# Performance work log

Measured on AMD Instinct MI355X. Metric: run time of the kernel, lower is better.

The kernel has to match this reference:

```python
import jax, jax.numpy as jnp
import numpy as np
import math

D_MODEL = 256
D_STATE = 16
D_CONV = 4
EXPAND = 2
N_HEADS = 4
D_INNER = EXPAND * D_MODEL          # 512
DT_RANK = (D_MODEL + 15) // 16      # 16
B_SZ, SEQ = 4, 2048


def setup_inputs() -> dict:
    key = jax.random.key(0)
    ks = jax.random.split(key, 12)
    rn = lambda i, shp, sc=0.02: jax.random.normal(ks[i], shp, dtype=jnp.float32) * sc
    x = jax.random.normal(ks[0], (B_SZ, SEQ, D_MODEL), dtype=jnp.float32)
    return dict(
        x=x,
        ln_g=jnp.ones((D_MODEL,), jnp.float32),
        ln_b=jnp.zeros((D_MODEL,), jnp.float32),
        W_in=rn(1, (D_MODEL, 2 * D_INNER)),
        conv_w=rn(2, (D_INNER, D_CONV), 0.1),
        conv_b=jnp.zeros((D_INNER,), jnp.float32),
        W_xproj=rn(3, (D_INNER, DT_RANK + 2 * D_STATE)),
        W_dt=rn(4, (DT_RANK, D_INNER), 0.1),
        b_dt=jnp.full((D_INNER,), -4.6, jnp.float32),  # softplus ~ 0.01 init
        A_log=jnp.log(jnp.tile(jnp.arange(1, D_STATE + 1, dtype=jnp.float32), (D_INNER, 1))),
        Dp=jnp.ones((D_INNER,), jnp.float32),
        W_out_m=rn(5, (D_INNER, D_MODEL)),
        W_qkv=rn(6, (D_MODEL, 3 * D_MODEL)),
        b_qkv=jnp.zeros((3 * D_MODEL,), jnp.float32),
        W_o=rn(7, (D_MODEL, D_MODEL)),
        b_o=jnp.zeros((D_MODEL,), jnp.float32),
        W_gate=rn(8, (2 * D_MODEL, D_MODEL)),
        b_gate=jnp.zeros((D_MODEL,), jnp.float32),
    )


def _sssd_forward(x, ln_g, ln_b, W_in, conv_w, conv_b, W_xproj, W_dt, b_dt,
                  A_log, Dp, W_out_m, W_qkv, b_qkv, W_o, b_o, W_gate, b_gate):
    B, L, D = x.shape
    # LayerNorm
    mu = x.mean(-1, keepdims=True)
    var = x.var(-1, keepdims=True)
    xn = (x - mu) * jax.lax.rsqrt(var + 1e-5) * ln_g + ln_b

    # ---- Mamba branch ----
    xz = xn @ W_in                      # (B,L,2*D_INNER)
    xm, z = jnp.split(xz, 2, axis=-1)
    # causal depthwise conv1d (kernel D_CONV)
    xp = jnp.pad(xm, ((0, 0), (D_CONV - 1, 0), (0, 0)))
    xc = conv_b + sum(xp[:, k:k + L, :] * conv_w[:, k] for k in range(D_CONV))
    xc = jax.nn.silu(xc)
    dbl = xc @ W_xproj                  # (B,L,DT_RANK+2*D_STATE)
    dt_in = dbl[..., :DT_RANK]
    Bm = dbl[..., DT_RANK:DT_RANK + D_STATE]
    Cm = dbl[..., DT_RANK + D_STATE:]
    dt = jax.nn.softplus(dt_in @ W_dt + b_dt)   # (B,L,D_INNER)
    A = -jnp.exp(A_log)                 # (D_INNER, D_STATE)

    def step(h, inp):
        x_t, dt_t, B_t, C_t = inp       # (B,Din),(B,Din),(B,N),(B,N)
        dA = jnp.exp(dt_t[..., None] * A)               # (B,Din,N)
        h = dA * h + (dt_t * x_t)[..., None] * B_t[:, None, :]
        y = jnp.einsum('bdn,bn->bd', h, C_t)
        return h, y

    h0 = jnp.zeros((B, D_INNER, D_STATE), x.dtype)
    xs = (jnp.swapaxes(xc, 0, 1), jnp.swapaxes(dt, 0, 1),
          jnp.swapaxes(Bm, 0, 1), jnp.swapaxes(Cm, 0, 1))
    _, ys = jax.lax.scan(step, h0, xs)
    y = jnp.swapaxes(ys, 0, 1) + xc * Dp
    y = y * jax.nn.silu(z)
    ssm_out = y @ W_out_m               # (B,L,D)

    # ---- MHSA branch (eval: no dropout) ----
    hd = D // N_HEADS
    qkv = xn @ W_qkv + b_qkv
    q, k, v = jnp.split(qkv, 3, axis=-1)
    sh = lambda t: t.reshape(B, L, N_HEADS, hd).transpose(0, 2, 1, 3)
    q, k, v = sh(q), sh(k), sh(v)
    scores = jnp.einsum('bhqd,bhkd->bhqk', q, k) * (1.0 / math.sqrt(hd))
    attn = jax.nn.softmax(scores, axis=-1)
    o = jnp.einsum('bhqk,bhkd->bhqd', attn, v).transpose(0, 2, 1, 3).reshape(B, L, D)
    attn_out = o @ W_o + b_o

    # ---- sigmoid gate fusion ----
    gate = jax.nn.sigmoid(jnp.concatenate([ssm_out, attn_out], axis=-1) @ W_gate + b_gate)
    fused = gate * ssm_out + (1.0 - gate) * attn_out
    return x + fused


def reference(x, ln_g, ln_b, W_in, conv_w, conv_b, W_xproj, W_dt, b_dt,
              A_log, Dp, W_out_m, W_qkv, b_qkv, W_o, b_o, W_gate, b_gate):
    return _sssd_forward(x, ln_g, ln_b, W_in, conv_w, conv_b, W_xproj, W_dt, b_dt,
                         A_log, Dp, W_out_m, W_qkv, b_qkv, W_o, b_o, W_gate, b_gate)
```

## Files before the change

kernel.cpp:

```cpp
#include <hip/hip_runtime.h>
#include <math.h>

#define B_SZ 4
#define SEQ 2048
#define DM 256
#define DI 512
#define DS 16
#define DTR 16
#define NH 4
#define HD 64
#define T_TOK (B_SZ*SEQ)
#define NCH 64
#define CL (SEQ/NCH)
#define NSP 4
#define QSCALE 0.18033688f

typedef short bf16x8 __attribute__((ext_vector_type(8)));
typedef float f32x4  __attribute__((ext_vector_type(4)));
typedef float f32x16 __attribute__((ext_vector_type(16)));
typedef unsigned short u16;

__device__ __forceinline__ float sigmoidf_(float x){ return 1.f/(1.f+__expf(-x)); }
__device__ __forceinline__ u16 f2bf(float x){
  unsigned int u = __float_as_uint(x);
  u += 0x7fffu + ((u>>16)&1u);
  return (u16)(u>>16);
}
__device__ __forceinline__ float bf2f(u16 u){ return __uint_as_float(((unsigned)u)<<16); }
__device__ __forceinline__ unsigned cvt_pk_bf16(float lo, float hi){
  unsigned r;
  asm("v_cvt_pk_bf16_f32 %0, %1, %2" : "=v"(r) : "v"(lo), "v"(hi));
  return r;
}
__device__ __forceinline__ void permswap(unsigned &a, unsigned &b){
  asm volatile("v_permlane32_swap_b32 %0, %1" : "+v"(a), "+v"(b));
}
__device__ __forceinline__ float xor32f(float v){
  unsigned a = __float_as_uint(v), b = a;
  permswap(a, b);
  return __uint_as_float(a);
}

struct TcvtArgs {
  const float* src[6];
  u16* dst[6];
  int K[6];
  int Nvalid[6];
  int Npad[6];
};
__global__ __launch_bounds__(256) void tcvt_all(TcvtArgs a) {
  int wi = blockIdx.z;
  int K = a.K[wi], Nv = a.Nvalid[wi], Np = a.Npad[wi];
  int k0 = blockIdx.x*64, n0 = blockIdx.y*64;
  if (k0 >= K || n0 >= Np) return;
  __shared__ u16 tile[64][65];
  const float* src = a.src[wi];
  u16* dst = a.dst[wi];
  int tn = threadIdx.x & 63, tq = threadIdx.x >> 6;
#pragma unroll
  for (int j=0;j<16;++j){
    int kk = j*4 + tq;
    int n = n0 + tn;
    tile[tn][kk] = (n < Nv) ? f2bf(src[(size_t)(k0+kk)*Nv + n]) : (u16)0;
  }
  __syncthreads();
#pragma unroll
  for (int j=0;j<16;++j){
    int nn = j*4 + tq;
    dst[(size_t)(n0+nn)*K + k0 + tn] = tile[nn][tn];
  }
}

__global__ __launch_bounds__(256) void ln_kernel(const float* __restrict__ x,
    const float* __restrict__ g, const float* __restrict__ b,
    u16* __restrict__ xn_bf) {
  int wid = threadIdx.x >> 6;
  int lane = threadIdx.x & 63;
  int token = blockIdx.x*4 + wid;
  const float* xr = x + (size_t)token*DM;
  float4 v = *(const float4*)&xr[lane*4];
  float s  = v.x+v.y+v.z+v.w;
  float ss = v.x*v.x+v.y*v.y+v.z*v.z+v.w*v.w;
  for (int m=1;m<64;m<<=1){ s += __shfl_xor(s,m); ss += __shfl_xor(ss,m); }
  float mu  = s * (1.f/DM);
  float var = ss*(1.f/DM) - mu*mu;
  float rs  = rsqrtf(var + 1e-5f);
  float4 gv = *(const float4*)&g[lane*4];
  float4 bv = *(const float4*)&b[lane*4];
  uint2 o;
  o.x = cvt_pk_bf16((v.x-mu)*rs*gv.x + bv.x, (v.y-mu)*rs*gv.y + bv.y);
  o.y = cvt_pk_bf16((v.z-mu)*rs*gv.z + bv.z, (v.w-mu)*rs*gv.w + bv.w);
  *(uint2*)&xn_bf[(size_t)token*DM + lane*4] = o;
}

template<int ACT>
__global__ __launch_bounds__(256) void gemm_mfma(const u16* __restrict__ A,
    const u16* __restrict__ Wt, const float* __restrict__ bias,
    float* __restrict__ C, u16* __restrict__ Cbf, int K, int ldc, int nvalid,
    int qcols, float qscale, const float* __restrict__ xres,
    const float* __restrict__ cat2, u16* __restrict__ vTout,
    u16* __restrict__ qkvout,
    const u16* __restrict__ A2, const u16* __restrict__ Wt2, int K2,
    const float* __restrict__ bias2) {
  __shared__ u16 lds[12288];
  int tid = threadIdx.x;
  int m0 = blockIdx.y*128;
  int n0 = blockIdx.x*64;
  const u16* Ap = A; const u16* Wp = Wt; int Kp = K; const float* bp = bias;
  int halfsel = 0;
  if (ACT==6){
    halfsel = (blockIdx.x >= 4);
    if (halfsel){ Ap = A2; Wp = Wt2; Kp = K2; bp = bias2; }
    n0 = (blockIdx.x & 3)*64;
  }
  int w = tid>>6, l = tid&63, lq = l&15, lg = l>>4;
  int wm = w>>1, wn = w&1;
  f32x4 acc[4][2] = {};
  for (int k0 = 0; k0 < Kp; k0 += 64) {
#pragma unroll
    for (int i=0;i<4;++i){
      int gid = i*256 + tid;
      int row = gid>>3, g = gid&7;
      *(bf16x8*)&lds[row*64 + ((g ^ (row&7))*8)] =
          *(const bf16x8*)&Ap[(size_t)(m0+row)*Kp + k0 + g*8];
    }
#pragma unroll
    for (int i=0;i<2;++i){
      int gid = i*256 + tid;
      int row = gid>>3, g = gid&7;
      *(bf16x8*)&lds[8192 + row*64 + ((g ^ (row&7))*8)] =
          *(const bf16x8*)&Wp[(size_t)(n0+row)*Kp + k0 + g*8];
    }
    __syncthreads();
#pragma unroll
    for (int ks=0;ks<2;++ks){
      bf16x8 af[4], bfv[2];
#pragma unroll
      for (int mi=0;mi<4;++mi){
        int row = wm*64 + mi*16 + lq;
        af[mi] = *(bf16x8*)&lds[row*64 + (((ks*4+lg) ^ (row&7))*8)];
      }
#pragma unroll
      for (int nj=0;nj<2;++nj){
        int row = wn*32 + nj*16 + lq;
        bfv[nj] = *(bf16x8*)&lds[8192 + row*64 + (((ks*4+lg) ^ (row&7))*8)];
      }
#pragma unroll
      for (int mi=0;mi<4;++mi)
#pragma unroll
        for (int nj=0;nj<2;++nj)
          acc[mi][nj] = __builtin_amdgcn_mfma_f32_16x16x32_bf16(af[mi], bfv[nj], acc[mi][nj], 0,0,0);
    }
    __syncthreads();
  }
#pragma unroll
  for (int mi=0;mi<4;++mi){
#pragma unroll
    for (int nj=0;nj<2;++nj){
#pragma unroll
      for (int r=0;r<4;++r){
        int row = m0 + wm*64 + mi*16 + lg*4 + r;
        int col = n0 + wn*32 + nj*16 + lq;
        if (col < nvalid) {
          float v = acc[mi][nj][r];
          if (ACT==0 && bias) v += bias[col];
          if (col < qcols) v *= qscale;
          if (ACT==2) {
            if (bias) v += bias[col];
            float g = sigmoidf_(v);
            float sv = cat2[(size_t)row*512 + col];
            float av = cat2[(size_t)row*512 + 256 + col];
            C[(size_t)row*256 + col] = xres[(size_t)row*256 + col] + g*sv + (1.f-g)*av;
          } else if (ACT==5) {
            if (col < 1024) {
              Cbf[(size_t)row*1024 + col] = f2bf(v);
            } else {
              int c2 = col - 1024;
              v += bias[c2];
              if (c2 < 256) v *= qscale;
              qkvout[(size_t)row*768 + c2] = f2bf(v);
              if (c2 >= 512) {
                int bb = row>>11, ll = row&2047;
                int hh = (c2-512)>>6, dd = (c2-512)&63;
                vTout[(((size_t)(bb*4+hh))*64 + dd)*SEQ + ll] = f2bf(v);
              }
            }
          } else if (ACT==6) {
            if (bp) v += bp[col];
            C[(size_t)row*512 + halfsel*256 + col] = v;
            Cbf[(size_t)row*512 + halfsel*256 + col] = f2bf(v);
          } else {
            if (C)   C[(size_t)row*ldc + col] = v;
            if (Cbf) Cbf[(size_t)row*ldc + col] = f2bf(v);
          }
        }
      }
    }
  }
}

__global__ __launch_bounds__(256) void conv_kernel(const u16* __restrict__ xzb,
    const float* __restrict__ cw, const float* __restrict__ cb,
    u16* __restrict__ xc_bf) {
  int idx = blockIdx.x*256 + threadIdx.x;
  int d2 = (idx & 255)*2;
  int t = idx >> 8;
  int l = t & (SEQ-1);
  float acc0 = cb[d2], acc1 = cb[d2+1];
  float4 wA = *(const float4*)&cw[d2*4];
  float4 wB = *(const float4*)&cw[d2*4+4];
  const u16* base = xzb + (size_t)t*1024 + d2;
  ushort2 v;
  if (l>=3){ v = *(const ushort2*)&base[-3*1024]; acc0 += bf2f(v.x)*wA.x; acc1 += bf2f(v.y)*wB.x; }
  if (l>=2){ v = *(const ushort2*)&base[-2*1024]; acc0 += bf2f(v.x)*wA.y; acc1 += bf2f(v.y)*wB.y; }
  if (l>=1){ v = *(const ushort2*)&base[-1*1024]; acc0 += bf2f(v.x)*wA.z; acc1 += bf2f(v.y)*wB.z; }
  v = *(const ushort2*)&base[0];
  acc0 += bf2f(v.x)*wA.w; acc1 += bf2f(v.y)*wB.w;
  float r0 = acc0 * sigmoidf_(acc0);
  float r1 = acc1 * sigmoidf_(acc1);
  *(unsigned*)&xc_bf[(size_t)t*DI + d2] = cvt_pk_bf16(r0, r1);
}

__global__ __launch_bounds__(256) void dt_kernel(const float* __restrict__ dbl,
    const float* __restrict__ Wdt, const float* __restrict__ bdt,
    u16* __restrict__ dt) {
  __shared__ float sdbl[4][16];
  int wid = threadIdx.x>>6, lane = threadIdx.x&63;
  int token = blockIdx.x*4 + wid;
  if (lane < 16) sdbl[wid][lane] = dbl[(size_t)token*48 + lane];
  __syncthreads();
  float din[16];
#pragma unroll
  for (int k=0;k<16;++k) din[k] = sdbl[wid][k];
#pragma unroll
  for (int r=0;r<8;++r){
    int d = lane + r*64;
    float acc = bdt[d];
#pragma unroll
    for (int k=0;k<16;++k) acc += din[k]*Wdt[k*DI+d];
    float sp = (acc > 20.f) ? acc : log1pf(__expf(acc));
    dt[(size_t)token*DI+d] = f2bf(sp);
  }
}

__global__ __launch_bounds__(512) void scan_p1(const u16* __restrict__ xc_bf,
    const u16* __restrict__ dt, const float* __restrict__ dbl,
    const float* __restrict__ A_log, u16* __restrict__ Pws, u16* __restrict__ Hws) {
  __shared__ float sB[CL][16];
  int d = threadIdx.x;
  int bc = blockIdx.x;
  int b = bc >> 6, c = bc & 63;
  {
    int t = threadIdx.x >> 4, n = threadIdx.x & 15;
    sB[t][n] = dbl[((size_t)b*SEQ + c*CL + t)*48 + DTR + n];
  }
  __syncthreads();
  float An[16];
#pragma unroll
  for (int i=0;i<4;++i){
    float4 a = *(const float4*)&A_log[d*16 + i*4];
    An[i*4+0] = -__expf(a.x); An[i*4+1] = -__expf(a.y);
    An[i*4+2] = -__expf(a.z); An[i*4+3] = -__expf(a.w);
  }
  float h[16] = {};
  float P[16];
#pragma unroll
  for (int n=0;n<16;++n) P[n] = 1.f;
  size_t tok = (size_t)b*SEQ + c*CL;
  for (int t=0;t<CL;++t,++tok){
    float dtv = bf2f(dt[tok*DI+d]);
    float xcv = bf2f(xc_bf[tok*DI+d]);
    float u = dtv*xcv;
    float4 B0 = *(float4*)&sB[t][0];
    float4 B1 = *(float4*)&sB[t][4];
    float4 B2 = *(float4*)&sB[t][8];
    float4 B3 = *(float4*)&sB[t][12];
    float Bv[16] = {B0.x,B0.y,B0.z,B0.w,B1.x,B1.y,B1.z,B1.w,
                    B2.x,B2.y,B2.z,B2.w,B3.x,B3.y,B3.z,B3.w};
#pragma unroll
    for (int n=0;n<16;++n){
      float e = __expf(dtv*An[n]);
      P[n] *= e;
      h[n] = e*h[n] + u*Bv[n];
    }
  }
  size_t base = (((size_t)b*NCH + c)*DI + d)*16;
#pragma unroll
  for (int i=0;i<8;++i){
    *(unsigned*)&Pws[base + i*2] = cvt_pk_bf16(P[i*2], P[i*2+1]);
    *(unsigned*)&Hws[base + i*2] = cvt_pk_bf16(h[i*2], h[i*2+1]);
  }
}

__global__ __launch_bounds__(256) void scan_combine(const u16* __restrict__ Pws,
    const u16* __restrict__ Hws, u16* __restrict__ H0ws) {
  int gid = blockIdx.x*256 + threadIdx.x;
  int b  = gid >> 13;
  int dn = gid & 8191;
  float h0 = 0.f;
#pragma unroll 4
  for (int c=0;c<NCH;++c){
    size_t idx = ((size_t)(b*NCH+c)<<13) + dn;
    H0ws[idx] = f2bf(h0);
    h0 = bf2f(Pws[idx])*h0 + bf2f(Hws[idx]);
  }
}

__global__ __launch_bounds__(512) void scan_p2(const u16* __restrict__ xc_bf,
    const u16* __restrict__ dt, const float* __restrict__ dbl,
    const float* __restrict__ A_log, const float* __restrict__ Dp,
    const u16* __restrict__ xzb, const u16* __restrict__ H0ws,
    u16* __restrict__ ygate_bf) {
  __shared__ float sBC[CL][32];
  int d = threadIdx.x;
  int bc = blockIdx.x;
  int b = bc >> 6, c = bc & 63;
#pragma unroll
  for (int i=0;i<2;++i){
    int idx = i*512 + threadIdx.x;
    int t = idx >> 5, q = idx & 31;
    sBC[t][q] = dbl[((size_t)b*SEQ + c*CL + t)*48 + DTR + q];
  }
  __syncthreads();
  float An[16];
#pragma unroll
  for (int i=0;i<4;++i){
    float4 a = *(const float4*)&A_log[d*16 + i*4];
    An[i*4+0] = -__expf(a.x); An[i*4+1] = -__expf(a.y);
    An[i*4+2] = -__expf(a.z); An[i*4+3] = -__expf(a.w);
  }
  float Dd = Dp[d];
  float h[16];
  size_t base = (((size_t)b*NCH + c)*DI + d)*16;
  {
    bf16x8 h8a = *(const bf16x8*)&H0ws[base];
    bf16x8 h8b = *(const bf16x8*)&H0ws[base+8];
#pragma unroll
    for (int n=0;n<8;++n){ h[n] = bf2f((u16)h8a[n]); h[8+n] = bf2f((u16)h8b[n]); }
  }
  size_t tok = (size_t)b*SEQ + c*CL;
  for (int t=0;t<CL;++t,++tok){
    float dtv = bf2f(dt[tok*DI+d]);
    float xcv = bf2f(xc_bf[tok*DI+d]);
    float zv  = bf2f(xzb[tok*1024 + DI + d]);
    float u = dtv*xcv;
    float4 B0 = *(float4*)&sBC[t][0];
    float4 B1 = *(float4*)&sBC[t][4];
    float4 B2 = *(float4*)&sBC[t][8];
    float4 B3 = *(float4*)&sBC[t][12];
    float4 C0 = *(float4*)&sBC[t][16];
    float4 C1 = *(float4*)&sBC[t][20];
    float4 C2 = *(float4*)&sBC[t][24];
    float4 C3 = *(float4*)&sBC[t][28];
    float Bv[16] = {B0.x,B0.y,B0.z,B0.w,B1.x,B1.y,B1.z,B1.w,
                    B2.x,B2.y,B2.z,B2.w,B3.x,B3.y,B3.z,B3.w};
    float Cv[16] = {C0.x,C0.y,C0.z,C0.w,C1.x,C1.y,C1.z,C1.w,
                    C2.x,C2.y,C2.z,C2.w,C3.x,C3.y,C3.z,C3.w};
    float y = 0.f;
#pragma unroll
    for (int n=0;n<16;++n){
      float e = __expf(dtv*An[n]);
      h[n] = e*h[n] + u*Bv[n];
      y += h[n]*Cv[n];
    }
    y += xcv*Dd;
    ygate_bf[tok*DI + d] = f2bf(y * (zv*sigmoidf_(zv)));
  }
}

__global__ __launch_bounds__(256) void attn_mfma_kernel(const u16* __restrict__ qkvb,
    const u16* __restrict__ vT,
    u16* __restrict__ Opart, float* __restrict__ ml) {
  int H = blockIdx.x + 8*blockIdx.y + 128*(int)blockIdx.z;
  int cx = H & 7, kk = H >> 3;
  int xq = kk & 7;
  int G  = cx*8 + (kk >> 3);
  int bh = G & 15, s = G >> 4;
  int b = bh>>2, h = bh&3;
  int tid = threadIdx.x;
  int w = tid>>6, l = tid&63;
  int lo32 = l & 31;
  int hi = l >> 5;
  size_t bbase = (size_t)b*SEQ;
  size_t vbase = (size_t)bh*HD*SEQ;
  int q_base = xq*256 + w*64;

  bf16x8 qf[2][4];
#pragma unroll
  for (int qg=0; qg<2; ++qg)
#pragma unroll
    for (int dsl=0; dsl<4; ++dsl)
      qf[qg][dsl] = *(const bf16x8*)&qkvb[(bbase + q_base + qg*32 + lo32)*768 + h*HD + dsl*16 + hi*8];

  float m_[2] = {-1e30f,-1e30f}, l_[2] = {0.f,0.f};
  f32x16 oacc[2][2] = {};

#define EXCH(X, Y, s_own, s_oth) { \
  unsigned xa = (X), yb = (Y); \
  permswap(xa, yb); \
  s_own = (l < 32) ? (X) : xa; \
  s_oth = (l < 32) ? yb : (Y); }

  for (int kt=s*8; kt<s*8+8; ++kt){
#pragma unroll
    for (int t32=0; t32<2; ++t32){
      const u16* kbase = &qkvb[(bbase + (size_t)kt*64 + t32*32 + lo32)*768 + 256 + h*HD + hi*8];
      bf16x8 kf[4];
#pragma unroll
      for (int dsl=0; dsl<4; ++dsl)
        kf[dsl] = *(const bf16x8*)&kbase[dsl*16];
      const u16* vb0 = &vT[vbase + (size_t)(lo32     )*SEQ + kt*64 + t32*32 + hi*8];
      const u16* vb1 = &vT[vbase + (size_t)(32 + lo32)*SEQ + kt*64 + t32*32 + hi*8];
      bf16x8 vf00 = *(const bf16x8*)&vb0[0];
      bf16x8 vf01 = *(const bf16x8*)&vb0[16];
      bf16x8 vf10 = *(const bf16x8*)&vb1[0];
      bf16x8 vf11 = *(const bf16x8*)&vb1[16];

      bf16x8 pf[2][2];
#pragma unroll
      for (int qg=0; qg<2; ++qg){
        f32x16 sacc = {0,0,0,0,0,0,0,0,0,0,0,0,0,0,0,0};
#pragma unroll
        for (int dsl=0; dsl<4; ++dsl)
          sacc = __builtin_amdgcn_mfma_f32_32x32x16_bf16(kf[dsl], qf[qg][dsl], sacc, 0,0,0);

        float tm = sacc[0];
#pragma unroll
        for (int r=1;r<16;++r) tm = fmaxf(tm, sacc[r]);
        tm = fmaxf(tm, xor32f(tm));
        if (__any(tm - m_[qg] > 8.f)) {
          float mn = fmaxf(m_[qg], tm);
          float sc = exp2f(m_[qg] - mn);
          m_[qg] = mn;
          l_[qg] *= sc;
#pragma unroll
          for (int r=0;r<16;++r){ oacc[qg][0][r] *= sc; oacc[qg][1][r] *= sc; }
        }
        float p[16];
        float ps = 0.f;
#pragma unroll
        for (int r=0;r<16;++r){ p[r] = exp2f(sacc[r] - m_[qg]); ps += p[r]; }
        ps += xor32f(ps);
        l_[qg] += ps;

        unsigned A0 = cvt_pk_bf16(p[0],p[1]),  A1 = cvt_pk_bf16(p[2],p[3]);
        unsigned B0 = cvt_pk_bf16(p[4],p[5]),  B1 = cvt_pk_bf16(p[6],p[7]);
        unsigned C0 = cvt_pk_bf16(p[8],p[9]),  C1 = cvt_pk_bf16(p[10],p[11]);
        unsigned D0 = cvt_pk_bf16(p[12],p[13]),D1 = cvt_pk_bf16(p[14],p[15]);
        unsigned s0,s1,s2,s3,s4,s5,s6,s7;
        EXCH(A0,B0,s0,s2); EXCH(A1,B1,s1,s3);
        EXCH(C0,D0,s4,s6); EXCH(C1,D1,s5,s7);
        ((unsigned*)&pf[qg][0])[0]=s0; ((unsigned*)&pf[qg][0])[1]=s1;
        ((unsigned*)&pf[qg][0])[2]=s2; ((unsigned*)&pf[qg][0])[3]=s3;
        ((unsigned*)&pf[qg][1])[0]=s4; ((unsigned*)&pf[qg][1])[1]=s5;
        ((unsigned*)&pf[qg][1])[2]=s6; ((unsigned*)&pf[qg][1])[3]=s7;
      }

      oacc[0][0] = __builtin_amdgcn_mfma_f32_32x32x16_bf16(vf00, pf[0][0], oacc[0][0], 0,0,0);
      oacc[0][0] = __builtin_amdgcn_mfma_f32_32x32x16_bf16(vf01, pf[0][1], oacc[0][0], 0,0,0);
      oacc[0][1] = __builtin_amdgcn_mfma_f32_32x32x16_bf16(vf10, pf[0][0], oacc[0][1], 0,0,0);
      oacc[0][1] = __builtin_amdgcn_mfma_f32_32x32x16_bf16(vf11, pf[0][1], oacc[0][1], 0,0,0);
      oacc[1][0] = __builtin_amdgcn_mfma_f32_32x32x16_bf16(vf00, pf[1][0], oacc[1][0], 0,0,0);
      oacc[1][0] = __builtin_amdgcn_mfma_f32_32x32x16_bf16(vf01, pf[1][1], oacc[1][0], 0,0,0);
      oacc[1][1] = __builtin_amdgcn_mfma_f32_32x32x16_bf16(vf10, pf[1][0], oacc[1][1], 0,0,0);
      oacc[1][1] = __builtin_amdgcn_mfma_f32_32x32x16_bf16(vf11, pf[1][1], oacc[1][1], 0,0,0);
    }
  }
#undef EXCH

  int sidx = bh*NSP + s;
#pragma unroll
  for (int qg=0; qg<2; ++qg){
    size_t rb = ((size_t)sidx*SEQ + q_base + qg*32 + lo32)*64;
#pragma unroll
    for (int dtile=0; dtile<2; ++dtile){
#pragma unroll
      for (int rg=0; rg<4; ++rg){
        uint2 pk;
        pk.x = cvt_pk_bf16(oacc[qg][dtile][rg*4+0], oacc[qg][dtile][rg*4+1]);
        pk.y = cvt_pk_bf16(oacc[qg][dtile][rg*4+2], oacc[qg][dtile][rg*4+3]);
        *(uint2*)&Opart[rb + dtile*32 + rg*8 + 4*hi] = pk;
      }
    }
    if (l < 32){
      ml[((size_t)sidx*SEQ + q_base + qg*32 + lo32)*2    ] = m_[qg];
      ml[((size_t)sidx*SEQ + q_base + qg*32 + lo32)*2 + 1] = l_[qg];
    }
  }
}

__global__ __launch_bounds__(256) void attn_merge_kernel(const u16* __restrict__ Opart,
    const float* __restrict__ ml, u16* __restrict__ attn_bf) {
  int w = threadIdx.x>>6, lane = threadIdx.x&63;
  int R = blockIdx.x*4 + w;
  int bh = R>>11, q = R&2047;
  float m[NSP], lv[NSP];
#pragma unroll
  for (int s=0;s<NSP;++s){
    m[s]  = ml[((size_t)(bh*NSP+s)*SEQ + q)*2];
    lv[s] = ml[((size_t)(bh*NSP+s)*SEQ + q)*2 + 1];
  }
  float ms = m[0];
#pragma unroll
  for (int s=1;s<NSP;++s) ms = fmaxf(ms, m[s]);
  float o = 0.f, lsum = 0.f;
#pragma unroll
  for (int s=0;s<NSP;++s){
    float wsc = exp2f(m[s]-ms);
    lsum += wsc*lv[s];
    o += wsc*bf2f(Opart[((size_t)(bh*NSP+s)*SEQ + q)*64 + lane]);
  }
  size_t token = (size_t)(bh>>2)*SEQ + q;
  attn_bf[token*DM + (bh&3)*HD + lane] = f2bf(o/lsum);
}

extern "C" void kernel_launch(void* const* d_in, const int* in_sizes, int n_in,
                              void* d_out, int out_size, void* d_ws, size_t ws_size,
                              hipStream_t stream) {
  const float* x      = (const float*)d_in[0];
  const float* ln_g   = (const float*)d_in[1];
  const float* ln_b   = (const float*)d_in[2];
  const float* W_in   = (const float*)d_in[3];
  const float* conv_w = (const float*)d_in[4];
  const float* conv_b = (const float*)d_in[5];
  const float* W_xproj= (const float*)d_in[6];
  const float* W_dt   = (const float*)d_in[7];
  const float* b_dt   = (const float*)d_in[8];
  const float* A_log  = (const float*)d_in[9];
  const float* Dp     = (const float*)d_in[10];
  const float* W_out_m= (const float*)d_in[11];
  const float* W_qkv  = (const float*)d_in[12];
  const float* b_qkv  = (const float*)d_in[13];
  const float* W_o    = (const float*)d_in[14];
  const float* b_o    = (const float*)d_in[15];
  const float* W_gate = (const float*)d_in[16];
  const float* b_gate = (const float*)d_in[17];
  float* out = (float*)d_out;

  float* ws = (float*)d_ws;
  u16*   xn_bf   = (u16*)(ws);
  u16*   xzb     = (u16*)(ws + 1048576);
  u16*   qkv_bf  = (u16*)(ws + 9437184);
  u16*   xc_bf   = (u16*)(ws + 12582912);
  float* dblb    = ws + 16777216;
  u16*   dtb     = (u16*)(ws + 17170432);
  u16*   ygate_bf= (u16*)(ws + 21364736);
  u16*   attn_bf = (u16*)(ws + 23461888);
  float* catb    = ws + 24510464;
  u16*   catb_bf = (u16*)(ws + 28704768);
  float* gateb   = ws + 30801920;
  u16*   Wt_all  = (u16*)(ws + 32899072);
  u16*   Opart = (u16*)(ws + 1048576);
  float* mlb   = (float*)xn_bf;
  u16*   vTb   = (u16*)gateb;
  u16*   Pws   = (u16*)catb;
  u16*   Hws   = (u16*)(catb + 1048576);
  u16*   H0ws  = (u16*)(catb + 2097152);

  u16* Wt_in   = Wt_all;
  u16* Wt_qkv  = Wt_all + 262144;
  u16* Wt_out  = Wt_all + 458752;
  u16* Wt_o    = Wt_all + 589824;
  u16* Wt_gate = Wt_all + 655360;
  u16* Wt_xp   = Wt_all + 786432;

  TcvtArgs ta;
  ta.src[0]=W_in;    ta.dst[0]=Wt_in;   ta.K[0]=256; ta.Nvalid[0]=1024; ta.Npad[0]=1024;
  ta.src[1]=W_qkv;   ta.dst[1]=Wt_qkv;  ta.K[1]=256; ta.Nvalid[1]=768;  ta.Npad[1]=768;
  ta.src[2]=W_out_m; ta.dst[2]=Wt_out;  ta.K[2]=512; ta.Nvalid[2]=256;  ta.Npad[2]=256;
  ta.src[3]=W_o;     ta.dst[3]=Wt_o;    ta.K[3]=256; ta.Nvalid[3]=256;  ta.Npad[3]=256;
  ta.src[4]=W_gate;  ta.dst[4]=Wt_gate; ta.K[4]=512; ta.Nvalid[4]=256;  ta.Npad[4]=256;
  ta.src[5]=W_xproj; ta.dst[5]=Wt_xp;   ta.K[5]=512; ta.Nvalid[5]=48;   ta.Npad[5]=64;
  tcvt_all<<<dim3(8,16,6), 256, 0, stream>>>(ta);

  ln_kernel<<<T_TOK/4, 256, 0, stream>>>(x, ln_g, ln_b, xn_bf);
  gemm_mfma<5><<<dim3(28,64), 256, 0, stream>>>(xn_bf, Wt_in, b_qkv, nullptr, xzb, 256, 0, 1792, 0, QSCALE, nullptr, nullptr, vTb, qkv_bf, nullptr, nullptr, 0, nullptr);
  conv_kernel<<<T_TOK, 256, 0, stream>>>(xzb, conv_w, conv_b, xc_bf);
  gemm_mfma<0><<<dim3(1,64), 256, 0, stream>>>(xc_bf, Wt_xp, nullptr, dblb, nullptr, 512, 48, 48, 0, 1.f, nullptr, nullptr, nullptr, nullptr, nullptr, nullptr, 0, nullptr);
  dt_kernel<<<T_TOK/4, 256, 0, stream>>>(dblb, W_dt, b_dt, dtb);
  scan_p1<<<B_SZ*NCH, 512, 0, stream>>>(xc_bf, dtb, dblb, A_log, Pws, Hws);
  scan_combine<<<128, 256, 0, stream>>>(Pws, Hws, H0ws);
  scan_p2<<<B_SZ*NCH, 512, 0, stream>>>(xc_bf, dtb, dblb, A_log, Dp, xzb, H0ws, ygate_bf);
  attn_mfma_kernel<<<dim3(8, 16, 4), 256, 0, stream>>>(qkv_bf, vTb, Opart, mlb);
  attn_merge_kernel<<<8192, 256, 0, stream>>>(Opart, mlb, attn_bf);
  gemm_mfma<6><<<dim3(8,64), 256, 0, stream>>>(ygate_bf, Wt_out, nullptr, catb, catb_bf, 512, 512, 256, 0, 1.f, nullptr, nullptr, nullptr, nullptr, attn_bf, Wt_o, 256, b_o);
  gemm_mfma<2><<<dim3(4,64), 256, 0, stream>>>(catb_bf, Wt_gate, b_gate, out, nullptr, 512, 256, 256, 0, 1.f, x, catb, nullptr, nullptr, nullptr, nullptr, 0, b_gate);
}
```

Measured before the change: 234.8 us.

## Fuse conv, x-projection and dt into one launch alongside attention

Replaces the separate conv, x-projection GEMM and dt kernels with a single pre-scan stage. Each of 128 blocks handles 64 tokens: it computes the causal conv and SiLU, stages the result in swizzled LDS, runs the x-projection with MFMA, then applies dt-projection and softplus. These blocks run in the same launch as the attention blocks (block index below 128 takes the SSM path), which cuts launch count and lets the SSM preprocessing overlap with attention. The attention partial outputs are moved into the catb workspace, which is only reused later by the scan. The 64KB static LDS array applies to every block, including attention blocks that never use it, which can limit occupancy. The conv loop inside each SSM block is also serial over 64 tokens.

Result: slower. 283.8 us (+20.9%).

```diff
diff --git a/kernel.cpp b/kernel.cpp
--- a/kernel.cpp
+++ b/kernel.cpp
@@ -163,7 +163,6 @@
         int col = n0 + wn*32 + nj*16 + lq;
         if (col < nvalid) {
           float v = acc[mi][nj][r];
-          if (ACT==0 && bias) v += bias[col];
           if (col < qcols) v *= qscale;
           if (ACT==2) {
             if (bias) v += bias[col];
@@ -189,9 +188,6 @@
             if (bp) v += bp[col];
             C[(size_t)row*512 + halfsel*256 + col] = v;
             Cbf[(size_t)row*512 + halfsel*256 + col] = f2bf(v);
-          } else {
-            if (C)   C[(size_t)row*ldc + col] = v;
-            if (Cbf) Cbf[(size_t)row*ldc + col] = f2bf(v);
           }
         }
       }
@@ -199,47 +195,202 @@
   }
 }
 
-__global__ __launch_bounds__(256) void conv_kernel(const u16* __restrict__ xzb,
-    const float* __restrict__ cw, const float* __restrict__ cb,
-    u16* __restrict__ xc_bf) {
-  int idx = blockIdx.x*256 + threadIdx.x;
-  int d2 = (idx & 255)*2;
-  int t = idx >> 8;
-  int l = t & (SEQ-1);
-  float acc0 = cb[d2], acc1 = cb[d2+1];
-  float4 wA = *(const float4*)&cw[d2*4];
-  float4 wB = *(const float4*)&cw[d2*4+4];
-  const u16* base = xzb + (size_t)t*1024 + d2;
-  ushort2 v;
-  if (l>=3){ v = *(const ushort2*)&base[-3*1024]; acc0 += bf2f(v.x)*wA.x; acc1 += bf2f(v.y)*wB.x; }
-  if (l>=2){ v = *(const ushort2*)&base[-2*1024]; acc0 += bf2f(v.x)*wA.y; acc1 += bf2f(v.y)*wB.y; }
-  if (l>=1){ v = *(const ushort2*)&base[-1*1024]; acc0 += bf2f(v.x)*wA.z; acc1 += bf2f(v.y)*wB.z; }
-  v = *(const ushort2*)&base[0];
-  acc0 += bf2f(v.x)*wA.w; acc1 += bf2f(v.y)*wB.w;
-  float r0 = acc0 * sigmoidf_(acc0);
-  float r1 = acc1 * sigmoidf_(acc1);
-  *(unsigned*)&xc_bf[(size_t)t*DI + d2] = cvt_pk_bf16(r0, r1);
-}
-
-__global__ __launch_bounds__(256) void dt_kernel(const float* __restrict__ dbl,
-    const float* __restrict__ Wdt, const float* __restrict__ bdt,
-    u16* __restrict__ dt) {
-  __shared__ float sdbl[4][16];
-  int wid = threadIdx.x>>6, lane = threadIdx.x&63;
-  int token = blockIdx.x*4 + wid;
-  if (lane < 16) sdbl[wid][lane] = dbl[(size_t)token*48 + lane];
-  __syncthreads();
-  float din[16];
-#pragma unroll
-  for (int k=0;k<16;++k) din[k] = sdbl[wid][k];
-#pragma unroll
-  for (int r=0;r<8;++r){
-    int d = lane + r*64;
-    float acc = bdt[d];
-#pragma unroll
-    for (int k=0;k<16;++k) acc += din[k]*Wdt[k*DI+d];
-    float sp = (acc > 20.f) ? acc : log1pf(__expf(acc));
-    dt[(size_t)token*DI+d] = f2bf(sp);
+__global__ __launch_bounds__(256) void attn_ssmpre_kernel(
+    const u16* __restrict__ qkvb, const u16* __restrict__ vT,
+    u16* __restrict__ Opart, float* __restrict__ ml,
+    const u16* __restrict__ xzb, const float* __restrict__ cw,
+    const float* __restrict__ cb, u16* __restrict__ xc_bf,
+    const u16* __restrict__ Wt_xp, const float* __restrict__ Wdt,
+    const float* __restrict__ bdt, float* __restrict__ dblb,
+    u16* __restrict__ dtb) {
+  __shared__ u16 xcs[32768];
+  __shared__ float dbls[64][16];
+  int tid = threadIdx.x;
+
+  if (blockIdx.x < 128) {
+    int bid = blockIdx.x;
+    int tok0 = bid*64;
+    for (int i=0;i<64;++i){
+      int t = i;
+      int d2 = tid*2;
+      int tg = tok0 + t;
+      int lpos = tg & (SEQ-1);
+      float acc0 = cb[d2], acc1 = cb[d2+1];
+      float4 wA = *(const float4*)&cw[d2*4];
+      float4 wB = *(const float4*)&cw[d2*4+4];
+      const u16* base = xzb + (size_t)tg*1024 + d2;
+      ushort2 v;
+      if (lpos>=3){ v = *(const ushort2*)&base[-3*1024]; acc0 += bf2f(v.x)*wA.x; acc1 += bf2f(v.y)*wB.x; }
+      if (lpos>=2){ v = *(const ushort2*)&base[-2*1024]; acc0 += bf2f(v.x)*wA.y; acc1 += bf2f(v.y)*wB.y; }
+      if (lpos>=1){ v = *(const ushort2*)&base[-1*1024]; acc0 += bf2f(v.x)*wA.z; acc1 += bf2f(v.y)*wB.z; }
+      v = *(const ushort2*)&base[0];
+      acc0 += bf2f(v.x)*wA.w; acc1 += bf2f(v.y)*wB.w;
+      float r0 = acc0 * sigmoidf_(acc0);
+      float r1 = acc1 * sigmoidf_(acc1);
+      unsigned pk = cvt_pk_bf16(r0, r1);
+      *(unsigned*)&xc_bf[(size_t)tg*DI + d2] = pk;
+      *(unsigned*)&xcs[t*512 + (((d2>>3) ^ (t&7))*8) + (d2&7)] = pk;
+    }
+    __syncthreads();
+    {
+      int w = tid>>6, l = tid&63, lq = l&15, lg = l>>4;
+      f32x4 acc[4] = {};
+      for (int ks=0; ks<16; ++ks){
+        int row = w*16 + lq;
+        int dcol = ks*32 + lg*8;
+        bf16x8 af = *(bf16x8*)&xcs[row*512 + (((dcol>>3) ^ (row&7))*8)];
+#pragma unroll
+        for (int nt=0; nt<4; ++nt){
+          int n = nt*16 + lq;
+          bf16x8 bfv = *(const bf16x8*)&Wt_xp[(size_t)n*512 + dcol];
+          acc[nt] = __builtin_amdgcn_mfma_f32_16x16x32_bf16(af, bfv, acc[nt], 0,0,0);
+        }
+      }
+#pragma unroll
+      for (int nt=0; nt<4; ++nt){
+#pragma unroll
+        for (int r=0;r<4;++r){
+          int t = w*16 + lg*4 + r;
+          int n = nt*16 + lq;
+          float v = acc[nt][r];
+          if (n < 48) dblb[(size_t)(tok0+t)*48 + n] = v;
+          if (nt == 0) dbls[t][lq] = v;
+        }
+      }
+    }
+    __syncthreads();
+    {
+      int d2 = tid*2;
+      float wdt0[16], wdt1[16];
+#pragma unroll
+      for (int k=0;k<16;++k){ wdt0[k] = Wdt[k*DI + d2]; wdt1[k] = Wdt[k*DI + d2 + 1]; }
+      float b0 = bdt[d2], b1 = bdt[d2+1];
+      for (int t=0;t<64;++t){
+        float a0 = b0, a1 = b1;
+#pragma unroll
+        for (int k=0;k<16;++k){ float dk = dbls[t][k]; a0 += dk*wdt0[k]; a1 += dk*wdt1[k]; }
+        float sp0 = (a0 > 20.f) ? a0 : log1pf(__expf(a0));
+        float sp1 = (a1 > 20.f) ? a1 : log1pf(__expf(a1));
+        *(unsigned*)&dtb[(size_t)(tok0+t)*DI + d2] = cvt_pk_bf16(sp0, sp1);
+      }
+    }
+    return;
+  }
+
+  int H = blockIdx.x - 128;
+  int cx = H & 7, kk = H >> 3;
+  int xq = kk & 7;
+  int G  = cx*8 + (kk >> 3);
+  int bh = G & 15, s = G >> 4;
+  int b = bh>>2, h = bh&3;
+  int w = tid>>6, l = tid&63;
+  int lo32 = l & 31;
+  int hi = l >> 5;
+  size_t bbase = (size_t)b*SEQ;
+  size_t vbase = (size_t)bh*HD*SEQ;
+  int q_base = xq*256 + w*64;
+
+  bf16x8 qf[2][4];
+#pragma unroll
+  for (int qg=0; qg<2; ++qg)
+#pragma unroll
+    for (int dsl=0; dsl<4; ++dsl)
+      qf[qg][dsl] = *(const bf16x8*)&qkvb[(bbase + q_base + qg*32 + lo32)*768 + h*HD + dsl*16 + hi*8];
+
+  float m_[2] = {-1e30f,-1e30f}, l_[2] = {0.f,0.f};
+  f32x16 oacc[2][2] = {};
+
+#define EXCH(X, Y, s_own, s_oth) { \
+  unsigned xa = (X), yb = (Y); \
+  permswap(xa, yb); \
+  s_own = (l < 32) ? (X) : xa; \
+  s_oth = (l < 32) ? yb : (Y); }
+
+  for (int kt=s*8; kt<s*8+8; ++kt){
+#pragma unroll
+    for (int t32=0; t32<2; ++t32){
+      const u16* kbase = &qkvb[(bbase + (size_t)kt*64 + t32*32 + lo32)*768 + 256 + h*HD + hi*8];
+      bf16x8 kf[4];
+#pragma unroll
+      for (int dsl=0; dsl<4; ++dsl)
+        kf[dsl] = *(const bf16x8*)&kbase[dsl*16];
+      const u16* vb0 = &vT[vbase + (size_t)(lo32     )*SEQ + kt*64 + t32*32 + hi*8];
+      const u16* vb1 = &vT[vbase + (size_t)(32 + lo32)*SEQ + kt*64 + t32*32 + hi*8];
+      bf16x8 vf00 = *(const bf16x8*)&vb0[0];
+      bf16x8 vf01 = *(const bf16x8*)&vb0[16];
+      bf16x8 vf10 = *(const bf16x8*)&vb1[0];
+      bf16x8 vf11 = *(const bf16x8*)&vb1[16];
+
+      bf16x8 pf[2][2];
+#pragma unroll
+      for (int qg=0; qg<2; ++qg){
+        f32x16 sacc = {0,0,0,0,0,0,0,0,0,0,0,0,0,0,0,0};
+#pragma unroll
+        for (int dsl=0; dsl<4; ++dsl)
+          sacc = __builtin_amdgcn_mfma_f32_32x32x16_bf16(kf[dsl], qf[qg][dsl], sacc, 0,0,0);
+
+        float tm = sacc[0];
+#pragma unroll
+        for (int r=1;r<16;++r) tm = fmaxf(tm, sacc[r]);
+        tm = fmaxf(tm, xor32f(tm));
+        if (__any(tm - m_[qg] > 8.f)) {
+          float mn = fmaxf(m_[qg], tm);
+          float sc = exp2f(m_[qg] - mn);
+          m_[qg] = mn;
+          l_[qg] *= sc;
+#pragma unroll
+          for (int r=0;r<16;++r){ oacc[qg][0][r] *= sc; oacc[qg][1][r] *= sc; }
+        }
+        float p[16];
+        float ps = 0.f;
+#pragma unroll
+        for (int r=0;r<16;++r){ p[r] = exp2f(sacc[r] - m_[qg]); ps += p[r]; }
+        ps += xor32f(ps);
+        l_[qg] += ps;
+
+        unsigned A0 = cvt_pk_bf16(p[0],p[1]),  A1 = cvt_pk_bf16(p[2],p[3]);
+        unsigned B0 = cvt_pk_bf16(p[4],p[5]),  B1 = cvt_pk_bf16(p[6],p[7]);
+        unsigned C0 = cvt_pk_bf16(p[8],p[9]),  C1 = cvt_pk_bf16(p[10],p[11]);
+        unsigned D0 = cvt_pk_bf16(p[12],p[13]),D1 = cvt_pk_bf16(p[14],p[15]);
+        unsigned s0,s1,s2,s3,s4,s5,s6,s7;
+        EXCH(A0,B0,s0,s2); EXCH(A1,B1,s1,s3);
+        EXCH(C0,D0,s4,s6); EXCH(C1,D1,s5,s7);
+        ((unsigned*)&pf[qg][0])[0]=s0; ((unsigned*)&pf[qg][0])[1]=s1;
+        ((unsigned*)&pf[qg][0])[2]=s2; ((unsigned*)&pf[qg][0])[3]=s3;
+        ((unsigned*)&pf[qg][1])[0]=s4; ((unsigned*)&pf[qg][1])[1]=s5;
+        ((unsigned*)&pf[qg][1])[2]=s6; ((unsigned*)&pf[qg][1])[3]=s7;
+      }
+
+      oacc[0][0] = __builtin_amdgcn_mfma_f32_32x32x16_bf16(vf00, pf[0][0], oacc[0][0], 0,0,0);
+      oacc[0][0] = __builtin_amdgcn_mfma_f32_32x32x16_bf16(vf01, pf[0][1], oacc[0][0], 0,0,0);
+      oacc[0][1] = __builtin_amdgcn_mfma_f32_32x32x16_bf16(vf10, pf[0][0], oacc[0][1], 0,0,0);
+      oacc[0][1] = __builtin_amdgcn_mfma_f32_32x32x16_bf16(vf11, pf[0][1], oacc[0][1], 0,0,0);
+      oacc[1][0] = __builtin_amdgcn_mfma_f32_32x32x16_bf16(vf00, pf[1][0], oacc[1][0], 0,0,0);
+      oacc[1][0] = __builtin_amdgcn_mfma_f32_32x32x16_bf16(vf01, pf[1][1], oacc[1][0], 0,0,0);
+      oacc[1][1] = __builtin_amdgcn_mfma_f32_32x32x16_bf16(vf10, pf[1][0], oacc[1][1], 0,0,0);
+      oacc[1][1] = __builtin_amdgcn_mfma_f32_32x32x16_bf16(vf11, pf[1][1], oacc[1][1], 0,0,0);
+    }
+  }
+#undef EXCH
+
+  int sidx = bh*NSP + s;
+#pragma unroll
+  for (int qg=0; qg<2; ++qg){
+    size_t rb = ((size_t)sidx*SEQ + q_base + qg*32 + lo32)*64;
+#pragma unroll
+    for (int dtile=0; dtile<2; ++dtile){
+#pragma unroll
+      for (int rg=0; rg<4; ++rg){
+        uint2 pk;
+        pk.x = cvt_pk_bf16(oacc[qg][dtile][rg*4+0], oacc[qg][dtile][rg*4+1]);
+        pk.y = cvt_pk_bf16(oacc[qg][dtile][rg*4+2], oacc[qg][dtile][rg*4+3]);
+        *(uint2*)&Opart[rb + dtile*32 + rg*8 + 4*hi] = pk;
+      }
+    }
+    if (l < 32){
+      ml[((size_t)sidx*SEQ + q_base + qg*32 + lo32)*2    ] = m_[qg];
+      ml[((size_t)sidx*SEQ + q_base + qg*32 + lo32)*2 + 1] = l_[qg];
+    }
   }
 }
 
@@ -365,127 +516,6 @@
     }
     y += xcv*Dd;
     ygate_bf[tok*DI + d] = f2bf(y * (zv*sigmoidf_(zv)));
-  }
-}
-
-__global__ __launch_bounds__(256) void attn_mfma_kernel(const u16* __restrict__ qkvb,
-    const u16* __restrict__ vT,
-    u16* __restrict__ Opart, float* __restrict__ ml) {
-  int H = blockIdx.x + 8*blockIdx.y + 128*(int)blockIdx.z;
-  int cx = H & 7, kk = H >> 3;
-  int xq = kk & 7;
-  int G  = cx*8 + (kk >> 3);
-  int bh = G & 15, s = G >> 4;
-  int b = bh>>2, h = bh&3;
-  int tid = threadIdx.x;
-  int w = tid>>6, l = tid&63;
-  int lo32 = l & 31;
-  int hi = l >> 5;
-  size_t bbase = (size_t)b*SEQ;
-  size_t vbase = (size_t)bh*HD*SEQ;
-  int q_base = xq*256 + w*64;
-
-  bf16x8 qf[2][4];
-#pragma unroll
-  for (int qg=0; qg<2; ++qg)
-#pragma unroll
-    for (int dsl=0; dsl<4; ++dsl)
-      qf[qg][dsl] = *(const bf16x8*)&qkvb[(bbase + q_base + qg*32 + lo32)*768 + h*HD + dsl*16 + hi*8];
-
-  float m_[2] = {-1e30f,-1e30f}, l_[2] = {0.f,0.f};
-  f32x16 oacc[2][2] = {};
-
-#define EXCH(X, Y, s_own, s_oth) { \
-  unsigned xa = (X), yb = (Y); \
-  permswap(xa, yb); \
-  s_own = (l < 32) ? (X) : xa; \
-  s_oth = (l < 32) ? yb : (Y); }
-
-  for (int kt=s*8; kt<s*8+8; ++kt){
-#pragma unroll
-    for (int t32=0; t32<2; ++t32){
-      const u16* kbase = &qkvb[(bbase + (size_t)kt*64 + t32*32 + lo32)*768 + 256 + h*HD + hi*8];
-      bf16x8 kf[4];
-#pragma unroll
-      for (int dsl=0; dsl<4; ++dsl)
-        kf[dsl] = *(const bf16x8*)&kbase[dsl*16];
-      const u16* vb0 = &vT[vbase + (size_t)(lo32     )*SEQ + kt*64 + t32*32 + hi*8];
-      const u16* vb1 = &vT[vbase + (size_t)(32 + lo32)*SEQ + kt*64 + t32*32 + hi*8];
-      bf16x8 vf00 = *(const bf16x8*)&vb0[0];
-      bf16x8 vf01 = *(const bf16x8*)&vb0[16];
-      bf16x8 vf10 = *(const bf16x8*)&vb1[0];
-      bf16x8 vf11 = *(const bf16x8*)&vb1[16];
-
-      bf16x8 pf[2][2];
-#pragma unroll
-      for (int qg=0; qg<2; ++qg){
-        f32x16 sacc = {0,0,0,0,0,0,0,0,0,0,0,0,0,0,0,0};
-#pragma unroll
-        for (int dsl=0; dsl<4; ++dsl)
-          sacc = __builtin_amdgcn_mfma_f32_32x32x16_bf16(kf[dsl], qf[qg][dsl], sacc, 0,0,0);
-
-        float tm = sacc[0];
-#pragma unroll
-        for (int r=1;r<16;++r) tm = fmaxf(tm, sacc[r]);
-        tm = fmaxf(tm, xor32f(tm));
-        if (__any(tm - m_[qg] > 8.f)) {
-          float mn = fmaxf(m_[qg], tm);
-          float sc = exp2f(m_[qg] - mn);
-          m_[qg] = mn;
-          l_[qg] *= sc;
-#pragma unroll
-          for (int r=0;r<16;++r){ oacc[qg][0][r] *= sc; oacc[qg][1][r] *= sc; }
-        }
-        float p[16];
-        float ps = 0.f;
-#pragma unroll
-        for (int r=0;r<16;++r){ p[r] = exp2f(sacc[r] - m_[qg]); ps += p[r]; }
-        ps += xor32f(ps);
-        l_[qg] += ps;
-
-        unsigned A0 = cvt_pk_bf16(p[0],p[1]),  A1 = cvt_pk_bf16(p[2],p[3]);
-        unsigned B0 = cvt_pk_bf16(p[4],p[5]),  B1 = cvt_pk_bf16(p[6],p[7]);
-        unsigned C0 = cvt_pk_bf16(p[8],p[9]),  C1 = cvt_pk_bf16(p[10],p[11]);
-        unsigned D0 = cvt_pk_bf16(p[12],p[13]),D1 = cvt_pk_bf16(p[14],p[15]);
-        unsigned s0,s1,s2,s3,s4,s5,s6,s7;
-        EXCH(A0,B0,s0,s2); EXCH(A1,B1,s1,s3);
-        EXCH(C0,D0,s4,s6); EXCH(C1,D1,s5,s7);
-        ((unsigned*)&pf[qg][0])[0]=s0; ((unsigned*)&pf[qg][0])[1]=s1;
-        ((unsigned*)&pf[qg][0])[2]=s2; ((unsigned*)&pf[qg][0])[3]=s3;
-        ((unsigned*)&pf[qg][1])[0]=s4; ((unsigned*)&pf[qg][1])[1]=s5;
-        ((unsigned*)&pf[qg][1])[2]=s6; ((unsigned*)&pf[qg][1])[3]=s7;
-      }
-
-      oacc[0][0] = __builtin_amdgcn_mfma_f32_32x32x16_bf16(vf00, pf[0][0], oacc[0][0], 0,0,0);
-      oacc[0][0] = __builtin_amdgcn_mfma_f32_32x32x16_bf16(vf01, pf[0][1], oacc[0][0], 0,0,0);
-      oacc[0][1] = __builtin_amdgcn_mfma_f32_32x32x16_bf16(vf10, pf[0][0], oacc[0][1], 0,0,0);
-      oacc[0][1] = __builtin_amdgcn_mfma_f32_32x32x16_bf16(vf11, pf[0][1], oacc[0][1], 0,0,0);
-      oacc[1][0] = __builtin_amdgcn_mfma_f32_32x32x16_bf16(vf00, pf[1][0], oacc[1][0], 0,0,0);
-      oacc[1][0] = __builtin_amdgcn_mfma_f32_32x32x16_bf16(vf01, pf[1][1], oacc[1][0], 0,0,0);
-      oacc[1][1] = __builtin_amdgcn_mfma_f32_32x32x16_bf16(vf10, pf[1][0], oacc[1][1], 0,0,0);
-      oacc[1][1] = __builtin_amdgcn_mfma_f32_32x32x16_bf16(vf11, pf[1][1], oacc[1][1], 0,0,0);
-    }
-  }
-#undef EXCH
-
-  int sidx = bh*NSP + s;
-#pragma unroll
-  for (int qg=0; qg<2; ++qg){
-    size_t rb = ((size_t)sidx*SEQ + q_base + qg*32 + lo32)*64;
-#pragma unroll
-    for (int dtile=0; dtile<2; ++dtile){
-#pragma unroll
-      for (int rg=0; rg<4; ++rg){
-        uint2 pk;
-        pk.x = cvt_pk_bf16(oacc[qg][dtile][rg*4+0], oacc[qg][dtile][rg*4+1]);
-        pk.y = cvt_pk_bf16(oacc[qg][dtile][rg*4+2], oacc[qg][dtile][rg*4+3]);
-        *(uint2*)&Opart[rb + dtile*32 + rg*8 + 4*hi] = pk;
-      }
-    }
-    if (l < 32){
-      ml[((size_t)sidx*SEQ + q_base + qg*32 + lo32)*2    ] = m_[qg];
-      ml[((size_t)sidx*SEQ + q_base + qg*32 + lo32)*2 + 1] = l_[qg];
-    }
   }
 }
 
@@ -550,7 +580,7 @@
   u16*   catb_bf = (u16*)(ws + 28704768);
   float* gateb   = ws + 30801920;
   u16*   Wt_all  = (u16*)(ws + 32899072);
-  u16*   Opart = (u16*)(ws + 1048576);
+  u16*   Opart = (u16*)catb;
   float* mlb   = (float*)xn_bf;
   u16*   vTb   = (u16*)gateb;
   u16*   Pws   = (u16*)catb;
@@ -575,14 +605,12 @@
 
   ln_kernel<<<T_TOK/4, 256, 0, stream>>>(x, ln_g, ln_b, xn_bf);
   gemm_mfma<5><<<dim3(28,64), 256, 0, stream>>>(xn_bf, Wt_in, b_qkv, nullptr, xzb, 256, 0, 1792, 0, QSCALE, nullptr, nullptr, vTb, qkv_bf, nullptr, nullptr, 0, nullptr);
-  conv_kernel<<<T_TOK, 256, 0, stream>>>(xzb, conv_w, conv_b, xc_bf);
-  gemm_mfma<0><<<dim3(1,64), 256, 0, stream>>>(xc_bf, Wt_xp, nullptr, dblb, nullptr, 512, 48, 48, 0, 1.f, nullptr, nullptr, nullptr, nullptr, nullptr, nullptr, 0, nullptr);
-  dt_kernel<<<T_TOK/4, 256, 0, stream>>>(dblb, W_dt, b_dt, dtb);
+  attn_ssmpre_kernel<<<640, 256, 0, stream>>>(qkv_bf, vTb, Opart, mlb,
+      xzb, conv_w, conv_b, xc_bf, Wt_xp, W_dt, b_dt, dblb, dtb);
+  attn_merge_kernel<<<8192, 256, 0, stream>>>(Opart, mlb, attn_bf);
   scan_p1<<<B_SZ*NCH, 512, 0, stream>>>(xc_bf, dtb, dblb, A_log, Pws, Hws);
   scan_combine<<<128, 256, 0, stream>>>(Pws, Hws, H0ws);
   scan_p2<<<B_SZ*NCH, 512, 0, stream>>>(xc_bf, dtb, dblb, A_log, Dp, xzb, H0ws, ygate_bf);
-  attn_mfma_kernel<<<dim3(8, 16, 4), 256, 0, stream>>>(qkv_bf, vTb, Opart, mlb);
-  attn_merge_kernel<<<8192, 256, 0, stream>>>(Opart, mlb, attn_bf);
   gemm_mfma<6><<<dim3(8,64), 256, 0, stream>>>(ygate_bf, Wt_out, nullptr, catb, catb_bf, 512, 512, 256, 0, 1.f, nullptr, nullptr, nullptr, nullptr, attn_bf, Wt_o, 256, b_o);
   gemm_mfma<2><<<dim3(4,64), 256, 0, stream>>>(catb_bf, Wt_gate, b_gate, out, nullptr, 512, 256, 256, 0, 1.f, x, catb, nullptr, nullptr, nullptr, nullptr, 0, b_gate);
 }
```
